# Kernel tuning notes

Hardware: AMD Instinct MI355X
Metric: run time of the kernel (lower is better)

## Reference

```python
import jax, jax.numpy as jnp
import numpy as np

N_P, E_P = 150000, 1200000   # protein nodes / edges (512 complexes batched)
N_L, E_L = 16000, 64000      # ligand nodes / edges
E_I = 400000                 # interaction (distance) edges, bidirectional
B, D, L = 512, 64, 3         # graphs, hidden_dim_g, num_g_layers
ND, ED = 58, 6               # initial node / edge feature dims


def edge_softmax(logits, dst, n):
    # softmax over incoming edges of each destination node
    m = jax.ops.segment_max(logits, dst, num_segments=n)
    ex = jnp.exp(logits - m[dst])
    s = jax.ops.segment_sum(ex, dst, num_segments=n)
    return ex / (s[dst] + 1e-9)


def gcn_layer(h, src, dst, W, n):
    # GraphConvolution: sum-aggregate neighbors, linear, relu, residual
    agg = jax.ops.segment_sum(h[src], dst, num_segments=n)
    return jax.nn.relu(agg @ W) + h


def gat_layer(h, e, src, dst, Wh, We, a_s, a_d, a_e, n):
    # GraphAttention (edge-feature aware GAT): additive attention logits,
    # edge-softmax by destination, weighted message sum, relu, residual.
    x = h @ Wh                      # [N, D]
    ee = e @ We                     # [E, D]
    logit = jax.nn.leaky_relu(
        (x[src] * a_s).sum(-1) + (x[dst] * a_d).sum(-1) + (ee * a_e).sum(-1), 0.2)
    alpha = edge_softmax(logit, dst, n)
    out = jax.ops.segment_sum(alpha[:, None] * (x[src] + ee), dst, num_segments=n)
    return jax.nn.relu(out) + h


def setup_inputs() -> dict:
    key = jax.random.key(0)
    ks = jax.random.split(key, 40)
    p = lambda k, shape: jax.random.normal(k, shape, jnp.float32) * 0.05
    h_p = jax.random.normal(ks[0], (N_P, ND), jnp.float32)
    e_p = jax.random.normal(ks[1], (E_P, ED), jnp.float32)
    src_p = jax.random.randint(ks[2], (E_P,), 0, N_P, jnp.int32)
    dst_p = jax.random.randint(ks[3], (E_P,), 0, N_P, jnp.int32)
    h_l = jax.random.normal(ks[4], (N_L, ND), jnp.float32)
    e_l = jax.random.normal(ks[5], (E_L, ED), jnp.float32)
    src_l = jax.random.randint(ks[6], (E_L,), 0, N_L, jnp.int32)
    dst_l = jax.random.randint(ks[7], (E_L,), 0, N_L, jnp.int32)
    coordinate = jax.random.normal(ks[8], (N_P + N_L, 3), jnp.float32) * 10.0
    # interaction edges: protein <-> ligand (ligand nodes offset by N_P)
    sp = jax.random.randint(ks[9], (E_I // 2,), 0, N_P, jnp.int32)
    dl = jax.random.randint(ks[10], (E_I // 2,), N_P, N_P + N_L, jnp.int32)
    src_i = jnp.concatenate([sp, dl])
    dst_i = jnp.concatenate([dl, sp])
    # graph ids for batched readout (balanced partition, monotone)
    gid_p = jnp.asarray(np.arange(N_P) * B // N_P, jnp.int32)
    gid_l = jnp.asarray(np.arange(N_L) * B // N_L, jnp.int32)
    gid_j = jnp.concatenate([gid_p, gid_l])
    return {
        'h_p': h_p, 'e_p': e_p, 'src_p': src_p, 'dst_p': dst_p,
        'h_l': h_l, 'e_l': e_l, 'src_l': src_l, 'dst_l': dst_l,
        'coordinate': coordinate, 'src_i': src_i, 'dst_i': dst_i, 'gid_j': gid_j,
        'Wn_p': p(ks[11], (ND, D)), 'We_p': p(ks[12], (ED, D)),
        'Wn_l': p(ks[13], (ND, D)), 'We_l': p(ks[14], (ED, D)),
        'Wemb_in': p(ks[15], (D, D)), 'Wemb_ie': p(ks[16], (1, D)),
        'Wc': p(ks[17], (L, D, D)),
        'Al_h': p(ks[18], (L, D, D)), 'Al_e': p(ks[19], (L, D, D)),
        'al_s': p(ks[20], (L, D)), 'al_d': p(ks[21], (L, D)), 'al_e': p(ks[22], (L, D)),
        'Ai_h': p(ks[23], (L, D, D)), 'Ai_e': p(ks[24], (L, D, D)),
        'ai_s': p(ks[25], (L, D)), 'ai_d': p(ks[26], (L, D)), 'ai_e': p(ks[27], (L, D)),
        'W1': p(ks[28], (D, D)), 'W2': p(ks[29], (D, 1)),
    }


def reference(h_p, e_p, src_p, dst_p, h_l, e_l, src_l, dst_l, coordinate,
              src_i, dst_i, gid_j, Wn_p, We_p, Wn_l, We_l, Wemb_in, Wemb_ie,
              Wc, Al_h, Al_e, al_s, al_d, al_e, Ai_h, Ai_e, ai_s, ai_d, ai_e,
              W1, W2):
    # node / edge embeddings (bias-free linears)
    hp = h_p @ Wn_p
    ep = e_p @ We_p
    hl = h_l @ Wn_l
    el = e_l @ We_l
    n_p, n_l = hp.shape[0], hl.shape[0]
    # protein branch: GraphConvolution stack
    for i in range(Wc.shape[0]):
        hp = gcn_layer(hp, src_p, dst_p, Wc[i], n_p)
    # ligand branch: GraphAttention stack (bond edge features)
    for i in range(Al_h.shape[0]):
        hl = gat_layer(hl, el, src_l, dst_l, Al_h[i], Al_e[i],
                       al_s[i], al_d[i], al_e[i], n_l)
    # join graphs: node states concatenated, edge feature = pair distance
    hj = jnp.concatenate([hp, hl], axis=0) @ Wemb_in          # [N_P+N_L, D]
    dist = jnp.sqrt(((coordinate[src_i] - coordinate[dst_i]) ** 2)
                    .sum(-1, keepdims=True) + 1e-12)           # [E_I, 1]
    vdw = dist @ Wemb_ie                                       # [E_I, D]
    n_j = n_p + n_l
    for i in range(Ai_h.shape[0]):
        hj = gat_layer(hj, vdw, src_i, dst_i, Ai_h[i], Ai_e[i],
                       ai_s[i], ai_d[i], ai_e[i], n_j)
    # sum readout per complex, then 2-layer bias-free MLP
    readout = jax.ops.segment_sum(hj, gid_j, num_segments=B)   # [B, D]
    return jax.nn.relu(readout @ W1) @ W2                      # [B, 1]
```

## Files before the change

### kernel.cpp

```cpp
#include <hip/hip_runtime.h>
#include <math.h>

#define THREADS 256

#define N_P 150000
#define E_P 1200000
#define N_L 16000
#define E_L 64000
#define E_I 400000
#define N_J (N_P + N_L)
#define NB  512
#define DIM 64
#define NLAYER 3
#define SCAN_TILE 1024

typedef float f4 __attribute__((ext_vector_type(4)));

static __device__ __forceinline__ float wred_sum(float v) {
    #pragma unroll
    for (int o = 32; o; o >>= 1) v += __shfl_xor(v, o);
    return v;
}
static __device__ __forceinline__ float gred_max(float v) {
    #pragma unroll
    for (int o = 1; o <= 8; o <<= 1) v = fmaxf(v, __shfl_xor(v, o));
    return v;
}
static __device__ __forceinline__ float gred_sum(float v) {
    #pragma unroll
    for (int o = 1; o <= 8; o <<= 1) v += __shfl_xor(v, o);
    return v;
}

__global__ void hist_k(const int* __restrict__ dst, int* __restrict__ cnt,
                       int* __restrict__ slot, int E)
{
    int e = blockIdx.x * THREADS + threadIdx.x;
    if (e >= E) return;
    slot[e] = atomicAdd(&cnt[dst[e]], 1);
}

__global__ void scan_local(const int* __restrict__ in, int* __restrict__ out,
                           int* __restrict__ partials, int n)
{
    __shared__ int lds[256];
    int t = threadIdx.x;
    int base = blockIdx.x * SCAN_TILE + t * 4;
    int v0 = base + 0 < n ? in[base + 0] : 0;
    int v1 = base + 1 < n ? in[base + 1] : 0;
    int v2 = base + 2 < n ? in[base + 2] : 0;
    int v3 = base + 3 < n ? in[base + 3] : 0;
    int s = v0 + v1 + v2 + v3;
    lds[t] = s;
    __syncthreads();
    #pragma unroll
    for (int off = 1; off < 256; off <<= 1) {
        int x = (t >= off) ? lds[t - off] : 0;
        __syncthreads();
        lds[t] += x;
        __syncthreads();
    }
    int excl = lds[t] - s;
    if (base + 0 < n) out[base + 0] = excl;
    if (base + 1 < n) out[base + 1] = excl + v0;
    if (base + 2 < n) out[base + 2] = excl + v0 + v1;
    if (base + 3 < n) out[base + 3] = excl + v0 + v1 + v2;
    if (t == 255) partials[blockIdx.x] = lds[255];
}

__global__ void scan_part(int* __restrict__ partials, int np)
{
    __shared__ int lds[256];
    int t = threadIdx.x;
    int v = t < np ? partials[t] : 0;
    lds[t] = v;
    __syncthreads();
    #pragma unroll
    for (int off = 1; off < 256; off <<= 1) {
        int x = (t >= off) ? lds[t - off] : 0;
        __syncthreads();
        lds[t] += x;
        __syncthreads();
    }
    if (t < np) partials[t] = lds[t] - v;
}

__global__ void scan_add(int* __restrict__ out, const int* __restrict__ partials,
                         int n, int etotal)
{
    int i = blockIdx.x * THREADS + threadIdx.x;
    if (i < n) out[i] += partials[i / SCAN_TILE];
    if (i == 0) out[n] = etotal;
}

__global__ void fill_p_k(const int* __restrict__ src, const int* __restrict__ dst,
                         const int* __restrict__ slot, const int* __restrict__ rp,
                         int* __restrict__ esrc, int E)
{
    int e = blockIdx.x * THREADS + threadIdx.x;
    if (e >= E) return;
    esrc[rp[dst[e]] + slot[e]] = src[e];
}

__global__ void fill_l_k(const int* __restrict__ src, const int* __restrict__ dst,
                         const int* __restrict__ slot, const int* __restrict__ rp,
                         int* __restrict__ esrc, int* __restrict__ eid, int E)
{
    int e = blockIdx.x * THREADS + threadIdx.x;
    if (e >= E) return;
    int pos = rp[dst[e]] + slot[e];
    esrc[pos] = src[e];
    eid[pos] = e;
}

__global__ void fill_i_k(const int* __restrict__ src, const int* __restrict__ dst,
                         const int* __restrict__ slot, const int* __restrict__ rp,
                         const float* __restrict__ coord,
                         int* __restrict__ esrc, float* __restrict__ dsorted, int E)
{
    int e = blockIdx.x * THREADS + threadIdx.x;
    if (e >= E) return;
    int s = src[e], d = dst[e];
    int pos = rp[d] + slot[e];
    esrc[pos] = s;
    float dx = coord[s * 3 + 0] - coord[d * 3 + 0];
    float dy = coord[s * 3 + 1] - coord[d * 3 + 1];
    float dz = coord[s * 3 + 2] - coord[d * 3 + 2];
    dsorted[pos] = sqrtf(dx * dx + dy * dy + dz * dz + 1e-12f);
}

template<int K, int EPI>
__global__ __launch_bounds__(256, 4)
void gemm64_k(const float* __restrict__ X, const float* __restrict__ W,
              const float* __restrict__ RES, const float* __restrict__ a1,
              const float* __restrict__ a2, float* __restrict__ Y,
              float* __restrict__ S1, float* __restrict__ S2, int N)
{
    __shared__ float Xs[64][68];
    __shared__ float Ws[K][64];
    int t = threadIdx.x;
    int tx = t & 15, ty = t >> 4;
    int rbase = blockIdx.x * 64;
    for (int i = t; i < K * 16; i += 256)
        *(f4*)&Ws[(i * 4) >> 6][(i * 4) & 63] = *(const f4*)&W[i * 4];
    if constexpr (K % 4 == 0) {
        #pragma unroll
        for (int j = t; j < 16 * K; j += 256) {
            int r = j / (K / 4), k4 = j % (K / 4);
            int row = rbase + r;
            f4 v = {0.f, 0.f, 0.f, 0.f};
            if (row < N) v = *(const f4*)&X[(long)row * K + k4 * 4];
            *(f4*)&Xs[r][k4 * 4] = v;
        }
    } else {
        for (int j = t; j < 64 * K; j += 256) {
            int r = j / K, k = j - r * K;
            int row = rbase + r;
            Xs[r][k] = (row < N) ? X[(long)row * K + k] : 0.f;
        }
    }
    __syncthreads();
    f4 acc[4] = {{0,0,0,0},{0,0,0,0},{0,0,0,0},{0,0,0,0}};
    #pragma unroll 4
    for (int k = 0; k < K; ++k) {
        f4 wv = *(const f4*)&Ws[k][tx * 4];
        #pragma unroll
        for (int i = 0; i < 4; ++i) {
            float xv = Xs[ty * 4 + i][k];
            acc[i] += wv * xv;
        }
    }
    #pragma unroll
    for (int i = 0; i < 4; ++i) {
        int row = rbase + ty * 4 + i;
        if (row >= N) continue;
        f4 y = acc[i];
        if constexpr (EPI == 1) {
            f4 res = *(const f4*)&RES[(long)row * DIM + tx * 4];
            #pragma unroll
            for (int c = 0; c < 4; ++c) y[c] = fmaxf(y[c], 0.f) + res[c];
        }
        *(f4*)&Y[(long)row * DIM + tx * 4] = y;
    }
    if constexpr (EPI == 2) {
        f4 a1v = *(const f4*)&a1[tx * 4];
        f4 a2v = *(const f4*)&a2[tx * 4];
        #pragma unroll
        for (int i = 0; i < 4; ++i) {
            float s = acc[i][0]*a1v[0] + acc[i][1]*a1v[1] + acc[i][2]*a1v[2] + acc[i][3]*a1v[3];
            float d = acc[i][0]*a2v[0] + acc[i][1]*a2v[1] + acc[i][2]*a2v[2] + acc[i][3]*a2v[3];
            #pragma unroll
            for (int o = 1; o <= 8; o <<= 1) {
                s += __shfl_xor(s, o);
                d += __shfl_xor(d, o);
            }
            int row = rbase + ty * 4 + i;
            if (tx == 0 && row < N) { S1[row] = s; S2[row] = d; }
        }
    }
    if constexpr (EPI == 3) {
        f4 a1v = *(const f4*)&a1[tx * 4];
        #pragma unroll
        for (int i = 0; i < 4; ++i) {
            float s = acc[i][0]*a1v[0] + acc[i][1]*a1v[1] + acc[i][2]*a1v[2] + acc[i][3]*a1v[3];
            #pragma unroll
            for (int o = 1; o <= 8; o <<= 1) s += __shfl_xor(s, o);
            int row = rbase + ty * 4 + i;
            if (tx == 0 && row < N) S1[row] = s;
        }
    }
}

__global__ __launch_bounds__(256, 4)
void gcn_fused_k(const float* __restrict__ Hin, const int* __restrict__ rp,
                 const int* __restrict__ esrc, const float* __restrict__ W,
                 float* __restrict__ Hout, int N)
{
    __shared__ float Xs[64][68];
    __shared__ float Ws[64][64];
    int t = threadIdx.x;
    int gl = t & 15, g = t >> 4, gw = (t & 63) >> 4;
    int rbase = blockIdx.x * 64;
    for (int i = t; i < 1024; i += 256)
        *(f4*)&Ws[(i * 4) >> 6][(i * 4) & 63] = *(const f4*)&W[i * 4];
    #pragma unroll
    for (int it = 0; it < 4; ++it) {
        int ln = g + it * 16;
        int node = rbase + ln;
        f4 acc = {0.f, 0.f, 0.f, 0.f};
        if (node < N) {
            int lo = rp[node], hi = rp[node + 1];
            for (int cb = lo; cb < hi; cb += 16) {
                int cnt = min(16, hi - cb);
                int sidx = (gl < cnt) ? esrc[cb + gl] : 0;
                for (int p = 0; p < cnt; ++p) {
                    int s = __shfl(sidx, gw * 16 + p);
                    acc += *(const f4*)&Hin[(long)s * DIM + gl * 4];
                }
            }
        }
        *(f4*)&Xs[ln][gl * 4] = acc;
    }
    __syncthreads();
    int tx = t & 15, ty = t >> 4;
    f4 acc[4] = {{0,0,0,0},{0,0,0,0},{0,0,0,0},{0,0,0,0}};
    #pragma unroll 4
    for (int k = 0; k < DIM; ++k) {
        f4 wv = *(const f4*)&Ws[k][tx * 4];
        #pragma unroll
        for (int i = 0; i < 4; ++i) {
            float xv = Xs[ty * 4 + i][k];
            acc[i] += wv * xv;
        }
    }
    #pragma unroll
    for (int i = 0; i < 4; ++i) {
        int row = rbase + ty * 4 + i;
        if (row >= N) continue;
        f4 res = *(const f4*)&Hin[(long)row * DIM + tx * 4];
        f4 y;
        #pragma unroll
        for (int c = 0; c < 4; ++c) y[c] = fmaxf(acc[i][c], 0.f) + res[c];
        *(f4*)&Hout[(long)row * DIM + tx * 4] = y;
    }
}

__global__ __launch_bounds__(256, 4)
void gat_l_k(const float* __restrict__ X, const float* __restrict__ Sn,
             const float* __restrict__ Dn, const float* __restrict__ Et,
             const float* __restrict__ EE, const int* __restrict__ rp,
             const int* __restrict__ esrc, const int* __restrict__ eid,
             float* __restrict__ H, int N)
{
    int t = threadIdx.x;
    int gl = t & 15, g = t >> 4, gw = (t & 63) >> 4;
    int node = blockIdx.x * 16 + g;
    int lo = 0, hi = 0;
    float dn = 0.f;
    if (node < N) { lo = rp[node]; hi = rp[node + 1]; dn = Dn[node]; }
    float m = -INFINITY, ssum = 0.f;
    f4 msg = {0.f, 0.f, 0.f, 0.f};
    for (int cb = lo; cb < hi; cb += 16) {
        int cnt = min(16, hi - cb);
        int sidx = 0, eidx = 0;
        float l = -INFINITY;
        if (gl < cnt) {
            sidx = esrc[cb + gl];
            eidx = eid[cb + gl];
            l = Sn[sidx] + dn + Et[eidx];
            l = (l >= 0.f) ? l : 0.2f * l;
        }
        float mnew = fmaxf(m, gred_max(l));
        float scale = expf(m - mnew);
        float ex = (gl < cnt) ? expf(l - mnew) : 0.f;
        ssum = ssum * scale + gred_sum(ex);
        msg *= scale;
        for (int p = 0; p < cnt; ++p) {
            float ep = __shfl(ex, gw * 16 + p);
            int s = __shfl(sidx, gw * 16 + p);
            int e = __shfl(eidx, gw * 16 + p);
            f4 xv = *(const f4*)&X[(long)s * DIM + gl * 4];
            f4 ev = *(const f4*)&EE[(long)e * DIM + gl * 4];
            msg += (xv + ev) * ep;
        }
        m = mnew;
    }
    float inv = 1.f / (ssum + 1e-9f);
    if (node < N) {
        long o = (long)node * DIM + gl * 4;
        f4 h = *(const f4*)&H[o];
        f4 r;
        #pragma unroll
        for (int c = 0; c < 4; ++c) r[c] = fmaxf(msg[c] * inv, 0.f) + h[c];
        *(f4*)&H[o] = r;
    }
}

__global__ __launch_bounds__(256, 4)
void gat_i_k(const float* __restrict__ X, const float* __restrict__ Sn,
             const float* __restrict__ Dn, const float* __restrict__ dsorted,
             const float* __restrict__ cbuf, const int* __restrict__ rp,
             const int* __restrict__ esrc, float* __restrict__ H, int N)
{
    int t = threadIdx.x;
    int gl = t & 15, g = t >> 4, gw = (t & 63) >> 4;
    int node = blockIdx.x * 16 + g;
    float ce = cbuf[64];
    int lo = 0, hi = 0;
    float dn = 0.f;
    if (node < N) { lo = rp[node]; hi = rp[node + 1]; dn = Dn[node]; }
    float m = -INFINITY, ssum = 0.f, wl = 0.f;
    f4 msg = {0.f, 0.f, 0.f, 0.f};
    for (int cb = lo; cb < hi; cb += 16) {
        int cnt = min(16, hi - cb);
        int sidx = 0;
        float dv = 0.f, l = -INFINITY;
        if (gl < cnt) {
            sidx = esrc[cb + gl];
            dv = dsorted[cb + gl];
            l = Sn[sidx] + dn + dv * ce;
            l = (l >= 0.f) ? l : 0.2f * l;
        }
        float mnew = fmaxf(m, gred_max(l));
        float scale = expf(m - mnew);
        float ex = (gl < cnt) ? expf(l - mnew) : 0.f;
        ssum = ssum * scale + gred_sum(ex);
        wl = wl * scale + ex * dv;
        msg *= scale;
        for (int p = 0; p < cnt; ++p) {
            float ep = __shfl(ex, gw * 16 + p);
            int s = __shfl(sidx, gw * 16 + p);
            msg += *(const f4*)&X[(long)s * DIM + gl * 4] * ep;
        }
        m = mnew;
    }
    float wsum = gred_sum(wl);
    float inv = 1.f / (ssum + 1e-9f);
    if (node < N) {
        long o = (long)node * DIM + gl * 4;
        f4 c4 = *(const f4*)&cbuf[gl * 4];
        f4 h = *(const f4*)&H[o];
        f4 r;
        #pragma unroll
        for (int c = 0; c < 4; ++c) {
            float v = (msg[c] + wsum * c4[c]) * inv;
            r[c] = fmaxf(v, 0.f) + h[c];
        }
        *(f4*)&H[o] = r;
    }
}

__global__ void cvec_all_k(const float* __restrict__ wie, const float* __restrict__ Ae,
                           const float* __restrict__ ae, float* __restrict__ cbuf)
{
    int L = blockIdx.x;
    int d = threadIdx.x;
    const float* A = Ae + (size_t)L * DIM * DIM;
    float c = 0.f;
    #pragma unroll
    for (int k = 0; k < DIM; ++k) c = fmaf(wie[k], A[k * DIM + d], c);
    cbuf[L * 80 + d] = c;
    float ce = wred_sum(c * ae[L * DIM + d]);
    if (d == 0) cbuf[L * 80 + 64] = ce;
}

__global__ __launch_bounds__(256, 1)
void readout_mlp_k(const float* __restrict__ HJ, const float* __restrict__ W1,
                   const float* __restrict__ W2, float* __restrict__ out)
{
    __shared__ float part[4][DIM];
    int t = threadIdx.x, wv = t >> 6, lane = t & 63;
    int b = blockIdx.x;
    float r = 0.f;
    long s0 = ((long)b * N_P + NB - 1) / NB;
    long e0 = ((long)(b + 1) * N_P + NB - 1) / NB;
    for (long n = s0 + wv; n < e0; n += 4) r += HJ[n * DIM + lane];
    long s1 = ((long)b * N_L + NB - 1) / NB;
    long e1 = ((long)(b + 1) * N_L + NB - 1) / NB;
    for (long n = s1 + wv; n < e1; n += 4) r += HJ[(N_P + n) * DIM + lane];
    part[wv][lane] = r;
    __syncthreads();
    if (wv != 0) return;
    r = part[0][lane] + part[1][lane] + part[2][lane] + part[3][lane];
    float acc = 0.f;
    #pragma unroll
    for (int k = 0; k < DIM; ++k) acc = fmaf(__shfl(r, k), W1[k * DIM + lane], acc);
    acc = fmaxf(acc, 0.f) * W2[lane];
    acc = wred_sum(acc);
    if (lane == 0) out[b] = acc;
}

extern "C" void kernel_launch(void* const* d_in, const int* in_sizes, int n_in,
                              void* d_out, int out_size, void* d_ws, size_t ws_size,
                              hipStream_t stream) {
    const float* h_p    = (const float*)d_in[0];
    const int*   src_p  = (const int*)d_in[2];
    const int*   dst_p  = (const int*)d_in[3];
    const float* h_l    = (const float*)d_in[4];
    const float* e_l    = (const float*)d_in[5];
    const int*   src_l  = (const int*)d_in[6];
    const int*   dst_l  = (const int*)d_in[7];
    const float* coord  = (const float*)d_in[8];
    const int*   src_i  = (const int*)d_in[9];
    const int*   dst_i  = (const int*)d_in[10];
    const float* Wn_p   = (const float*)d_in[12];
    const float* Wn_l   = (const float*)d_in[14];
    const float* We_l   = (const float*)d_in[15];
    const float* Wemb_in= (const float*)d_in[16];
    const float* Wemb_ie= (const float*)d_in[17];
    const float* Wc     = (const float*)d_in[18];
    const float* Al_h   = (const float*)d_in[19];
    const float* Al_e   = (const float*)d_in[20];
    const float* al_s   = (const float*)d_in[21];
    const float* al_d   = (const float*)d_in[22];
    const float* al_e   = (const float*)d_in[23];
    const float* Ai_h   = (const float*)d_in[24];
    const float* Ai_e   = (const float*)d_in[25];
    const float* ai_s   = (const float*)d_in[26];
    const float* ai_d   = (const float*)d_in[27];
    const float* ai_e   = (const float*)d_in[28];
    const float* W1     = (const float*)d_in[29];
    const float* W2     = (const float*)d_in[30];
    float* out = (float*)d_out;

    char* ws = (char*)d_ws;
    auto alloc = [&](size_t bytes) -> void* {
        char* p = ws;
        ws += (bytes + 255) & ~(size_t)255;
        return (void*)p;
    };
    float* HP    = (float*)alloc((size_t)N_P * DIM * 4);
    float* HL    = (float*)alloc((size_t)N_L * DIM * 4);
    float* EL    = (float*)alloc((size_t)E_L * DIM * 4);
    float* EE    = (float*)alloc((size_t)E_L * DIM * 4);
    float* HJ    = (float*)alloc((size_t)N_J * DIM * 4);
    float* XJ    = (float*)alloc((size_t)N_J * DIM * 4);
    float* SN    = (float*)alloc((size_t)N_J * 4);
    float* DN    = (float*)alloc((size_t)N_J * 4);
    float* ET    = (float*)alloc((size_t)E_L * 4);
    int*   cnt_p = (int*)alloc((size_t)N_P * 4);
    int*   cnt_l = (int*)alloc((size_t)N_L * 4);
    int*   cnt_i = (int*)alloc((size_t)N_J * 4);
    int*   rp_p  = (int*)alloc((size_t)(N_P + 1) * 4);
    int*   rp_l  = (int*)alloc((size_t)(N_L + 1) * 4);
    int*   rp_i  = (int*)alloc((size_t)(N_J + 1) * 4);
    int*   slot  = (int*)alloc((size_t)E_P * 4);
    int*   esrc_p= (int*)alloc((size_t)E_P * 4);
    int*   esrc_l= (int*)alloc((size_t)E_L * 4);
    int*   eid_l = (int*)alloc((size_t)E_L * 4);
    int*   esrc_i= (int*)alloc((size_t)E_I * 4);
    float* dsort = (float*)alloc((size_t)E_I * 4);
    int*   parts = (int*)alloc(256 * 4);
    float* CBUF  = (float*)alloc(3 * 80 * 4);
    (void)ws_size; (void)in_sizes; (void)n_in; (void)out_size;

    auto cdiv = [](int a, int b) { return (a + b - 1) / b; };

    hipMemsetAsync(cnt_p, 0, (size_t)N_P * 4, stream);
    hipMemsetAsync(cnt_l, 0, (size_t)N_L * 4, stream);
    hipMemsetAsync(cnt_i, 0, (size_t)N_J * 4, stream);
    auto build = [&](const int* dst, int* cnt, int* rp, int E, int N) {
        hist_k<<<cdiv(E, THREADS), THREADS, 0, stream>>>(dst, cnt, slot, E);
        int nb = cdiv(N, SCAN_TILE);
        scan_local<<<nb, 256, 0, stream>>>(cnt, rp, parts, N);
        scan_part<<<1, 256, 0, stream>>>(parts, nb);
        scan_add<<<cdiv(N, THREADS), THREADS, 0, stream>>>(rp, parts, N, E);
    };
    build(dst_p, cnt_p, rp_p, E_P, N_P);
    fill_p_k<<<cdiv(E_P, THREADS), THREADS, 0, stream>>>(src_p, dst_p, slot, rp_p, esrc_p, E_P);
    build(dst_l, cnt_l, rp_l, E_L, N_L);
    fill_l_k<<<cdiv(E_L, THREADS), THREADS, 0, stream>>>(src_l, dst_l, slot, rp_l, esrc_l, eid_l, E_L);
    build(dst_i, cnt_i, rp_i, E_I, N_J);
    fill_i_k<<<cdiv(E_I, THREADS), THREADS, 0, stream>>>(src_i, dst_i, slot, rp_i, coord, esrc_i, dsort, E_I);

    cvec_all_k<<<3, 64, 0, stream>>>(Wemb_ie, Ai_e, ai_e, CBUF);

    gemm64_k<58, 0><<<cdiv(N_P, 64), THREADS, 0, stream>>>(h_p, Wn_p, nullptr, nullptr, nullptr,
                                                           HP, nullptr, nullptr, N_P);
    gemm64_k<58, 0><<<cdiv(N_L, 64), THREADS, 0, stream>>>(h_l, Wn_l, nullptr, nullptr, nullptr,
                                                           HL, nullptr, nullptr, N_L);
    gemm64_k<6, 0><<<cdiv(E_L, 64), THREADS, 0, stream>>>(e_l, We_l, nullptr, nullptr, nullptr,
                                                          EL, nullptr, nullptr, E_L);

    for (int i = 0; i < NLAYER; ++i) {
        const float* Wh = Al_h + (size_t)i * DIM * DIM;
        const float* We = Al_e + (size_t)i * DIM * DIM;
        gemm64_k<64, 2><<<cdiv(N_L, 64), THREADS, 0, stream>>>(HL, Wh, nullptr,
                                                               al_s + i * DIM, al_d + i * DIM,
                                                               XJ, SN, DN, N_L);
        gemm64_k<64, 3><<<cdiv(E_L, 64), THREADS, 0, stream>>>(EL, We, nullptr,
                                                               al_e + i * DIM, nullptr,
                                                               EE, ET, nullptr, E_L);
        gat_l_k<<<cdiv(N_L, 16), THREADS, 0, stream>>>(XJ, SN, DN, ET, EE, rp_l, esrc_l,
                                                       eid_l, HL, N_L);
    }

    float* pin = HP;
    float* pout = XJ;
    for (int i = 0; i < NLAYER; ++i) {
        gcn_fused_k<<<cdiv(N_P, 64), THREADS, 0, stream>>>(pin, rp_p, esrc_p,
                                                           Wc + (size_t)i * DIM * DIM, pout, N_P);
        float* tmp = pin; pin = pout; pout = tmp;
    }

    gemm64_k<64, 0><<<cdiv(N_P, 64), THREADS, 0, stream>>>(pin, Wemb_in, nullptr, nullptr, nullptr,
                                                           HJ, nullptr, nullptr, N_P);
    gemm64_k<64, 0><<<cdiv(N_L, 64), THREADS, 0, stream>>>(HL, Wemb_in, nullptr, nullptr, nullptr,
                                                           HJ + (size_t)N_P * DIM, nullptr, nullptr, N_L);

    for (int i = 0; i < NLAYER; ++i) {
        const float* Wh = Ai_h + (size_t)i * DIM * DIM;
        gemm64_k<64, 2><<<cdiv(N_J, 64), THREADS, 0, stream>>>(HJ, Wh, nullptr,
                                                               ai_s + i * DIM, ai_d + i * DIM,
                                                               XJ, SN, DN, N_J);
        gat_i_k<<<cdiv(N_J, 16), THREADS, 0, stream>>>(XJ, SN, DN, dsort, CBUF + i * 80, rp_i,
                                                       esrc_i, HJ, N_J);
    }

    readout_mlp_k<<<NB, THREADS, 0, stream>>>(HJ, W1, W2, out);
}
```

Before: 791.2 us.

## Read weights from global instead of LDS, raise occupancy, fuse embedding GEMM into last GCN

```diff
diff --git a/kernel.cpp b/kernel.cpp
--- a/kernel.cpp
+++ b/kernel.cpp
@@ -130,19 +130,16 @@
 }
 
 template<int K, int EPI>
-__global__ __launch_bounds__(256, 4)
+__global__ __launch_bounds__(256, 8)
 void gemm64_k(const float* __restrict__ X, const float* __restrict__ W,
               const float* __restrict__ RES, const float* __restrict__ a1,
               const float* __restrict__ a2, float* __restrict__ Y,
               float* __restrict__ S1, float* __restrict__ S2, int N)
 {
     __shared__ float Xs[64][68];
-    __shared__ float Ws[K][64];
     int t = threadIdx.x;
     int tx = t & 15, ty = t >> 4;
     int rbase = blockIdx.x * 64;
-    for (int i = t; i < K * 16; i += 256)
-        *(f4*)&Ws[(i * 4) >> 6][(i * 4) & 63] = *(const f4*)&W[i * 4];
     if constexpr (K % 4 == 0) {
         #pragma unroll
         for (int j = t; j < 16 * K; j += 256) {
@@ -163,7 +160,7 @@
     f4 acc[4] = {{0,0,0,0},{0,0,0,0},{0,0,0,0},{0,0,0,0}};
     #pragma unroll 4
     for (int k = 0; k < K; ++k) {
-        f4 wv = *(const f4*)&Ws[k][tx * 4];
+        f4 wv = *(const f4*)&W[k * DIM + tx * 4];
         #pragma unroll
         for (int i = 0; i < 4; ++i) {
             float xv = Xs[ty * 4 + i][k];
@@ -211,18 +208,16 @@
     }
 }
 
-__global__ __launch_bounds__(256, 4)
+template<int JOIN>
+__global__ __launch_bounds__(256, 8)
 void gcn_fused_k(const float* __restrict__ Hin, const int* __restrict__ rp,
                  const int* __restrict__ esrc, const float* __restrict__ W,
-                 float* __restrict__ Hout, int N)
+                 const float* __restrict__ W2, float* __restrict__ Hout, int N)
 {
     __shared__ float Xs[64][68];
-    __shared__ float Ws[64][64];
     int t = threadIdx.x;
     int gl = t & 15, g = t >> 4, gw = (t & 63) >> 4;
     int rbase = blockIdx.x * 64;
-    for (int i = t; i < 1024; i += 256)
-        *(f4*)&Ws[(i * 4) >> 6][(i * 4) & 63] = *(const f4*)&W[i * 4];
     #pragma unroll
     for (int it = 0; it < 4; ++it) {
         int ln = g + it * 16;
@@ -246,26 +241,56 @@
     f4 acc[4] = {{0,0,0,0},{0,0,0,0},{0,0,0,0},{0,0,0,0}};
     #pragma unroll 4
     for (int k = 0; k < DIM; ++k) {
-        f4 wv = *(const f4*)&Ws[k][tx * 4];
+        f4 wv = *(const f4*)&W[k * DIM + tx * 4];
         #pragma unroll
         for (int i = 0; i < 4; ++i) {
             float xv = Xs[ty * 4 + i][k];
             acc[i] += wv * xv;
         }
     }
+    f4 yv[4];
     #pragma unroll
     for (int i = 0; i < 4; ++i) {
         int row = rbase + ty * 4 + i;
-        if (row >= N) continue;
-        f4 res = *(const f4*)&Hin[(long)row * DIM + tx * 4];
-        f4 y;
-        #pragma unroll
-        for (int c = 0; c < 4; ++c) y[c] = fmaxf(acc[i][c], 0.f) + res[c];
-        *(f4*)&Hout[(long)row * DIM + tx * 4] = y;
-    }
-}
-
-__global__ __launch_bounds__(256, 4)
+        if (row < N) {
+            f4 res = *(const f4*)&Hin[(long)row * DIM + tx * 4];
+            #pragma unroll
+            for (int c = 0; c < 4; ++c) yv[i][c] = fmaxf(acc[i][c], 0.f) + res[c];
+        } else {
+            yv[i] = f4{0.f, 0.f, 0.f, 0.f};
+        }
+    }
+    if constexpr (JOIN == 0) {
+        #pragma unroll
+        for (int i = 0; i < 4; ++i) {
+            int row = rbase + ty * 4 + i;
+            if (row < N) *(f4*)&Hout[(long)row * DIM + tx * 4] = yv[i];
+        }
+    } else {
+        __syncthreads();
+        #pragma unroll
+        for (int i = 0; i < 4; ++i)
+            *(f4*)&Xs[ty * 4 + i][tx * 4] = yv[i];
+        __syncthreads();
+        f4 acc2[4] = {{0,0,0,0},{0,0,0,0},{0,0,0,0},{0,0,0,0}};
+        #pragma unroll 4
+        for (int k = 0; k < DIM; ++k) {
+            f4 wv = *(const f4*)&W2[k * DIM + tx * 4];
+            #pragma unroll
+            for (int i = 0; i < 4; ++i) {
+                float xv = Xs[ty * 4 + i][k];
+                acc2[i] += wv * xv;
+            }
+        }
+        #pragma unroll
+        for (int i = 0; i < 4; ++i) {
+            int row = rbase + ty * 4 + i;
+            if (row < N) *(f4*)&Hout[(long)row * DIM + tx * 4] = acc2[i];
+        }
+    }
+}
+
+__global__ __launch_bounds__(256, 8)
 void gat_l_k(const float* __restrict__ X, const float* __restrict__ Sn,
              const float* __restrict__ Dn, const float* __restrict__ Et,
              const float* __restrict__ EE, const int* __restrict__ rp,
@@ -316,7 +341,7 @@
     }
 }
 
-__global__ __launch_bounds__(256, 4)
+__global__ __launch_bounds__(256, 8)
 void gat_i_k(const float* __restrict__ X, const float* __restrict__ Sn,
              const float* __restrict__ Dn, const float* __restrict__ dsorted,
              const float* __restrict__ cbuf, const int* __restrict__ rp,
@@ -515,16 +540,13 @@
                                                        eid_l, HL, N_L);
     }
 
-    float* pin = HP;
-    float* pout = XJ;
-    for (int i = 0; i < NLAYER; ++i) {
-        gcn_fused_k<<<cdiv(N_P, 64), THREADS, 0, stream>>>(pin, rp_p, esrc_p,
-                                                           Wc + (size_t)i * DIM * DIM, pout, N_P);
-        float* tmp = pin; pin = pout; pout = tmp;
-    }
-
-    gemm64_k<64, 0><<<cdiv(N_P, 64), THREADS, 0, stream>>>(pin, Wemb_in, nullptr, nullptr, nullptr,
-                                                           HJ, nullptr, nullptr, N_P);
+    gcn_fused_k<0><<<cdiv(N_P, 64), THREADS, 0, stream>>>(HP, rp_p, esrc_p,
+                                                          Wc + 0 * DIM * DIM, nullptr, XJ, N_P);
+    gcn_fused_k<0><<<cdiv(N_P, 64), THREADS, 0, stream>>>(XJ, rp_p, esrc_p,
+                                                          Wc + 1 * (size_t)DIM * DIM, nullptr, HP, N_P);
+    gcn_fused_k<1><<<cdiv(N_P, 64), THREADS, 0, stream>>>(HP, rp_p, esrc_p,
+                                                          Wc + 2 * (size_t)DIM * DIM, Wemb_in, HJ, N_P);
+
     gemm64_k<64, 0><<<cdiv(N_L, 64), THREADS, 0, stream>>>(HL, Wemb_in, nullptr, nullptr, nullptr,
                                                            HJ + (size_t)N_P * DIM, nullptr, nullptr, N_L);
 
```

New measurement: 814.1 us. 1.03x slower.
